# Kernel tuning notes

Measured on AMD Instinct MI355X. Metric: run time of the kernel, lower is better.

The kernel has to match this reference:

```python
import jax, jax.numpy as jnp
import numpy as np

# Genotype structure constants (see init_kwargs)
N_NODES = 100_000   # total nodes in topological order
N_IN = 1024         # first N_IN nodes are input-layer nodes (copy x)
N_OUT = 1024        # last N_OUT nodes are output-layer nodes
FAN_IN = 32         # predecessors per non-input node
BATCH = 128


def setup_inputs() -> dict:
    key = jax.random.key(0)
    k1, k2, k3 = jax.random.split(key, 3)
    x = jax.random.normal(k1, (BATCH, N_IN), dtype=jnp.float32)
    weights = jax.random.normal(k2, (N_NODES, FAN_IN), dtype=jnp.float32) * 0.5
    # predecessor ids: node i may only read nodes with index < i (topological DAG)
    raw = np.asarray(jax.random.randint(k3, (N_NODES, FAN_IN), 0, N_NODES))
    lim = np.maximum(np.arange(N_NODES), 1)[:, None]
    in_ids = jnp.asarray((raw % lim).astype(np.int32))
    return {"x": x, "weights": weights, "in_ids": in_ids}


def reference(x, weights, in_ids):
    B, n_in = x.shape
    n_nodes, _ = weights.shape
    # vals[i] holds the output of node i for every batch element: [N, B]
    vals = jnp.zeros((n_nodes, B), dtype=x.dtype).at[:n_in].set(x.T)
    node_idx = jnp.arange(n_in, n_nodes)

    def step(vals, inp):
        i, ids, w = inp
        gathered = vals[ids]                      # [K, B] predecessor outputs
        out = jax.nn.relu(jnp.einsum('k,kb->b', w, gathered))  # linear (no bias) + ReLU
        return vals.at[i].set(out), None

    vals, _ = jax.lax.scan(step, vals, (node_idx, in_ids[n_in:], weights[n_in:]))
    # stack output-layer node values -> [B, N_OUT]
    return vals[n_nodes - N_OUT:].T
```

## Files before the change

kernel.cpp:

```cpp
#include <hip/hip_runtime.h>
#include <hip/hip_fp16.h>


#define N_NODES 100000
#define N_IN    1024
#define N_OUT   1024
#define FAN_IN  32
#define NPAIR   64
#define N_TODO  (N_NODES - N_IN)
#define SENTW   0xFFFFFFFFu
#define NW      2048
#define NBLK    (NW / 4)
#define PGSZ    1024
#define PGSHIFT 10
#define NPAGES  ((N_TODO + PGSZ - 1) / PGSZ)

#define OFS_WM    4096
#define OFS_PC    8192
#define PC_STRIDE 64
#define OFS_VALS  65536

__global__ __launch_bounds__(256) void init_kernel(const float* __restrict__ x,
                                                   unsigned* __restrict__ vals,
                                                   int* __restrict__ wm_page,
                                                   int* __restrict__ page_cnt) {
    const int tid = blockIdx.x * blockDim.x + threadIdx.x;
    if (tid == 0) *wm_page = 0;
    if (tid < NPAGES) page_cnt[tid * PC_STRIDE] = 0;
    if (tid < N_IN * NPAIR) {
        const int i = tid >> 6;
        const int b = tid & 63;
        __half2 h2 = __floats2half2_rn(x[b * N_IN + i], x[(b + 64) * N_IN + i]);
        vals[i * NPAIR + b] = *reinterpret_cast<unsigned*>(&h2);
    }
    uint4* p = (uint4*)(vals + (size_t)N_IN * NPAIR);
    const int total = N_TODO * NPAIR / 4;
    const uint4 s4 = make_uint4(SENTW, SENTW, SENTW, SENTW);
    for (int t = tid; t < total; t += gridDim.x * blockDim.x)
        p[t] = s4;
}

__device__ __forceinline__ void wm_advance(int* wm_page, int* page_cnt) {
    for (;;) {
        int cur = __hip_atomic_load(wm_page, __ATOMIC_RELAXED,
                                    __HIP_MEMORY_SCOPE_AGENT);
        if (cur >= NPAGES) break;
        int fps = min(PGSZ, N_TODO - (cur << PGSHIFT));
        int cnt = __hip_atomic_load(page_cnt + (size_t)cur * PC_STRIDE,
                                    __ATOMIC_RELAXED, __HIP_MEMORY_SCOPE_AGENT);
        if (cnt < fps) break;
        int expected = cur;
        __hip_atomic_compare_exchange_strong(wm_page, &expected, cur + 1,
                                             __ATOMIC_RELAXED, __ATOMIC_RELAXED,
                                             __HIP_MEMORY_SCOPE_AGENT);
    }
}

__global__ __launch_bounds__(256, 2) void dag_kernel(const float* __restrict__ weights,
                                                     const int* __restrict__ in_ids,
                                                     unsigned* __restrict__ vals,
                                                     int* __restrict__ wm_page,
                                                     int* __restrict__ page_cnt,
                                                     float* __restrict__ out) {
    const int tid  = threadIdx.x;
    const int lane = tid & 63;
    const int w    = __builtin_amdgcn_readfirstlane(blockIdx.x * 4 + (tid >> 6));

    unsigned v[FAN_IN];
    unsigned vn[FAN_IN];
    unsigned wmv  = 0;
    unsigned cohm = 0, cmn = 0;
    int pend_pg = -1, pend_old = 0;

    int node = N_IN + w;

    {
        const long wb = (long)node * FAN_IN;
#pragma unroll
        for (int k = 0; k < FAN_IN; ++k) {
            const int id = in_ids[wb + k];
            const unsigned* p = vals + (long)id * NPAIR + lane;
            if (id < N_IN) {
                asm volatile("global_load_dword %0, %1, off"
                             : "=v"(vn[k]) : "v"(p));
            } else {
                asm volatile("global_load_dword %0, %1, off sc0 sc1"
                             : "=v"(vn[k]) : "v"(p));
                cmn |= 1u << k;
            }
        }
        asm volatile("global_load_dword %0, %1, off sc0 sc1"
                     : "=v"(wmv) : "v"(wm_page));
    }

    for (;;) {
        asm volatile("s_waitcnt vmcnt(0)" ::: "memory");
        __builtin_amdgcn_sched_barrier(0);

#pragma unroll
        for (int k = 0; k < FAN_IN; ++k) v[k] = vn[k];
        cohm = cmn;

        if (pend_pg >= 0) {
            if (lane == 0) {
                const int ps = min(PGSZ, N_TODO - (pend_pg << PGSHIFT));
                if (pend_old + 1 == ps) wm_advance(wm_page, page_cnt);
            }
            pend_pg = -1;
        }
        if (node - NW >= N_IN) {
            const int ppg = (node - NW - N_IN) >> PGSHIFT;
            if (lane == 0)
                pend_old = __hip_atomic_fetch_add(page_cnt + (size_t)ppg * PC_STRIDE, 1,
                                                  __ATOMIC_RELAXED,
                                                  __HIP_MEMORY_SCOPE_AGENT);
            pend_pg = ppg;
        }

        const int wmn = __builtin_amdgcn_readfirstlane((int)(N_IN + (wmv << PGSHIFT)));

        const int nxt = node + NW;
        cmn = 0;
        if (nxt < N_NODES) {
            const long wbn = (long)nxt * FAN_IN;
#pragma unroll
            for (int k = 0; k < FAN_IN; ++k) {
                const int id = in_ids[wbn + k];
                const unsigned* p = vals + (long)id * NPAIR + lane;
                if (id < wmn) {
                    asm volatile("global_load_dword %0, %1, off"
                                 : "=v"(vn[k]) : "v"(p));
                } else {
                    asm volatile("global_load_dword %0, %1, off sc0 sc1"
                                 : "=v"(vn[k]) : "v"(p));
                    cmn |= 1u << k;
                }
            }
            asm volatile("global_load_dword %0, %1, off sc0 sc1"
                         : "=v"(wmv) : "v"(wm_page));
        }

        const long wb = (long)node * FAN_IN;

        unsigned need = cohm;
        while (need) {
            unsigned got = 0;
#pragma unroll
            for (int k = 0; k < FAN_IN; ++k)
                if ((need >> k) & 1u)
                    if (__all(v[k] != SENTW)) got |= 1u << k;
            need &= ~got;
            if (!need) break;
            __builtin_amdgcn_s_sleep(1);
#pragma unroll
            for (int k = 0; k < FAN_IN; ++k)
                if ((need >> k) & 1u) {
                    const int id = in_ids[wb + k];
                    v[k] = __hip_atomic_load(vals + (long)id * NPAIR + lane,
                                             __ATOMIC_RELAXED,
                                             __HIP_MEMORY_SCOPE_AGENT);
                }
        }

        float acc0 = 0.f, acc1 = 0.f;
#pragma unroll
        for (int k = 0; k < FAN_IN; ++k) {
            const float  wk = weights[wb + k];
            const __half2 h2 = *reinterpret_cast<const __half2*>(&v[k]);
            const float2  f  = __half22float2(h2);
            acc0 = fmaf(wk, f.x, acc0);
            acc1 = fmaf(wk, f.y, acc1);
        }
        acc0 = fmaxf(acc0, 0.f);
        acc1 = fmaxf(acc1, 0.f);

        __half2 hr = __floats2half2_rn(acc0, acc1);
        const unsigned ow = *reinterpret_cast<const unsigned*>(&hr);
        unsigned* orow = vals + (long)node * NPAIR + lane;
        asm volatile("global_store_dword %0, %1, off sc0 sc1"
                     :: "v"(orow), "v"(ow));

        if (node >= N_NODES - N_OUT) {
            const int jo = node - (N_NODES - N_OUT);
            out[lane * N_OUT + jo]        = acc0;
            out[(lane + 64) * N_OUT + jo] = acc1;
        }

        if (nxt >= N_NODES) break;
        node = nxt;
    }

    asm volatile("s_waitcnt vmcnt(0)" ::: "memory");
    if (lane == 0) {
        if (pend_pg >= 0) {
            const int ps = min(PGSZ, N_TODO - (pend_pg << PGSHIFT));
            if (pend_old + 1 == ps) wm_advance(wm_page, page_cnt);
        }
        const int pg = (node - N_IN) >> PGSHIFT;
        const int ps = min(PGSZ, N_TODO - (pg << PGSHIFT));
        int old = __hip_atomic_fetch_add(page_cnt + (size_t)pg * PC_STRIDE, 1,
                                         __ATOMIC_RELAXED, __HIP_MEMORY_SCOPE_AGENT);
        if (old + 1 == ps) wm_advance(wm_page, page_cnt);
    }
}

extern "C" void kernel_launch(void* const* d_in, const int* in_sizes, int n_in,
                              void* d_out, int out_size, void* d_ws, size_t ws_size,
                              hipStream_t stream) {
    const float* x       = (const float*)d_in[0];
    const float* weights = (const float*)d_in[1];
    const int*   in_ids  = (const int*)d_in[2];
    float*       out     = (float*)d_out;

    int*      wm_page = (int*)((char*)d_ws + OFS_WM);
    int*      page_cnt= (int*)((char*)d_ws + OFS_PC);
    unsigned* vals    = (unsigned*)((char*)d_ws + OFS_VALS);

    init_kernel<<<2048, 256, 0, stream>>>(x, vals, wm_page, page_cnt);
    dag_kernel<<<NBLK, 256, 0, stream>>>(weights, in_ids, vals,
                                         wm_page, page_cnt, out);
}
```

Before: 564.5 us.

## Split page completion counters into sub-counters and replicate the watermark

Each page's single completion counter becomes 32 cache-line-padded sub-counters, one per wave group (w mod 32). A per-page subs_done counter records finished sub-counters, and the watermark advances only when all 32 are done. The watermark is also copied to 32 padded replicas that blocks poll by block index. This spreads atomic traffic and polling loads that all hit one address across many addresses. In exchange it adds a second atomic level, 31 extra stores on each watermark advance, and a larger workspace footprint.

New measurement: 524.7 us. -7.1%, faster.

```diff
diff --git a/kernel.cpp b/kernel.cpp
--- a/kernel.cpp
+++ b/kernel.cpp
@@ -14,19 +14,28 @@
 #define PGSZ    1024
 #define PGSHIFT 10
 #define NPAGES  ((N_TODO + PGSZ - 1) / PGSZ)
+#define NSUB    32
+#define WMREP   32
 
 #define OFS_WM    4096
-#define OFS_PC    8192
-#define PC_STRIDE 64
-#define OFS_VALS  65536
+#define OFS_SD    16384
+#define OFS_SUB   65536
+#define OFS_VALS  860160
+#define LSTRIDE   64
+
+__device__ __forceinline__ int subq(int pg) {
+    return min(PGSZ, N_TODO - (pg << PGSHIFT)) >> 5;
+}
 
 __global__ __launch_bounds__(256) void init_kernel(const float* __restrict__ x,
                                                    unsigned* __restrict__ vals,
-                                                   int* __restrict__ wm_page,
-                                                   int* __restrict__ page_cnt) {
+                                                   int* __restrict__ wm,
+                                                   int* __restrict__ subs_done,
+                                                   int* __restrict__ sub_cnt) {
     const int tid = blockIdx.x * blockDim.x + threadIdx.x;
-    if (tid == 0) *wm_page = 0;
-    if (tid < NPAGES) page_cnt[tid * PC_STRIDE] = 0;
+    if (tid < WMREP)        wm[tid * LSTRIDE] = 0;
+    if (tid < NPAGES)       subs_done[tid * LSTRIDE] = 0;
+    if (tid < NPAGES * NSUB) sub_cnt[tid * LSTRIDE] = 0;
     if (tid < N_IN * NPAIR) {
         const int i = tid >> 6;
         const int b = tid & 63;
@@ -40,31 +49,36 @@
         p[t] = s4;
 }
 
-__device__ __forceinline__ void wm_advance(int* wm_page, int* page_cnt) {
+__device__ __forceinline__ void wm_advance(int* wm, int* subs_done) {
     for (;;) {
-        int cur = __hip_atomic_load(wm_page, __ATOMIC_RELAXED,
-                                    __HIP_MEMORY_SCOPE_AGENT);
+        int cur = __hip_atomic_load(wm, __ATOMIC_RELAXED, __HIP_MEMORY_SCOPE_AGENT);
         if (cur >= NPAGES) break;
-        int fps = min(PGSZ, N_TODO - (cur << PGSHIFT));
-        int cnt = __hip_atomic_load(page_cnt + (size_t)cur * PC_STRIDE,
-                                    __ATOMIC_RELAXED, __HIP_MEMORY_SCOPE_AGENT);
-        if (cnt < fps) break;
+        int sd = __hip_atomic_load(subs_done + (size_t)cur * LSTRIDE,
+                                   __ATOMIC_RELAXED, __HIP_MEMORY_SCOPE_AGENT);
+        if (sd < NSUB) break;
         int expected = cur;
-        __hip_atomic_compare_exchange_strong(wm_page, &expected, cur + 1,
+        __hip_atomic_compare_exchange_strong(wm, &expected, cur + 1,
                                              __ATOMIC_RELAXED, __ATOMIC_RELAXED,
                                              __HIP_MEMORY_SCOPE_AGENT);
     }
+    int fin = __hip_atomic_load(wm, __ATOMIC_RELAXED, __HIP_MEMORY_SCOPE_AGENT);
+    for (int r = 1; r < WMREP; ++r)
+        __hip_atomic_store(wm + (size_t)r * LSTRIDE, fin,
+                           __ATOMIC_RELAXED, __HIP_MEMORY_SCOPE_AGENT);
 }
 
 __global__ __launch_bounds__(256, 2) void dag_kernel(const float* __restrict__ weights,
                                                      const int* __restrict__ in_ids,
                                                      unsigned* __restrict__ vals,
-                                                     int* __restrict__ wm_page,
-                                                     int* __restrict__ page_cnt,
+                                                     int* __restrict__ wm,
+                                                     int* __restrict__ subs_done,
+                                                     int* __restrict__ sub_cnt,
                                                      float* __restrict__ out) {
     const int tid  = threadIdx.x;
     const int lane = tid & 63;
     const int w    = __builtin_amdgcn_readfirstlane(blockIdx.x * 4 + (tid >> 6));
+    const int g    = w & (NSUB - 1);
+    int* wm_rep    = wm + (size_t)(blockIdx.x & (WMREP - 1)) * LSTRIDE;
 
     unsigned v[FAN_IN];
     unsigned vn[FAN_IN];
@@ -90,7 +104,7 @@
             }
         }
         asm volatile("global_load_dword %0, %1, off sc0 sc1"
-                     : "=v"(wmv) : "v"(wm_page));
+                     : "=v"(wmv) : "v"(wm_rep));
     }
 
     for (;;) {
@@ -102,18 +116,19 @@
         cohm = cmn;
 
         if (pend_pg >= 0) {
-            if (lane == 0) {
-                const int ps = min(PGSZ, N_TODO - (pend_pg << PGSHIFT));
-                if (pend_old + 1 == ps) wm_advance(wm_page, page_cnt);
+            if (lane == 0 && pend_old + 1 == subq(pend_pg)) {
+                int sd = __hip_atomic_fetch_add(subs_done + (size_t)pend_pg * LSTRIDE, 1,
+                                                __ATOMIC_RELAXED, __HIP_MEMORY_SCOPE_AGENT);
+                if (sd + 1 == NSUB) wm_advance(wm, subs_done);
             }
             pend_pg = -1;
         }
         if (node - NW >= N_IN) {
             const int ppg = (node - NW - N_IN) >> PGSHIFT;
             if (lane == 0)
-                pend_old = __hip_atomic_fetch_add(page_cnt + (size_t)ppg * PC_STRIDE, 1,
-                                                  __ATOMIC_RELAXED,
-                                                  __HIP_MEMORY_SCOPE_AGENT);
+                pend_old = __hip_atomic_fetch_add(
+                    sub_cnt + ((size_t)ppg * NSUB + g) * LSTRIDE, 1,
+                    __ATOMIC_RELAXED, __HIP_MEMORY_SCOPE_AGENT);
             pend_pg = ppg;
         }
 
@@ -137,7 +152,7 @@
                 }
             }
             asm volatile("global_load_dword %0, %1, off sc0 sc1"
-                         : "=v"(wmv) : "v"(wm_page));
+                         : "=v"(wmv) : "v"(wm_rep));
         }
 
         const long wb = (long)node * FAN_IN;
@@ -192,15 +207,19 @@
 
     asm volatile("s_waitcnt vmcnt(0)" ::: "memory");
     if (lane == 0) {
-        if (pend_pg >= 0) {
-            const int ps = min(PGSZ, N_TODO - (pend_pg << PGSHIFT));
-            if (pend_old + 1 == ps) wm_advance(wm_page, page_cnt);
+        if (pend_pg >= 0 && pend_old + 1 == subq(pend_pg)) {
+            int sd = __hip_atomic_fetch_add(subs_done + (size_t)pend_pg * LSTRIDE, 1,
+                                            __ATOMIC_RELAXED, __HIP_MEMORY_SCOPE_AGENT);
+            if (sd + 1 == NSUB) wm_advance(wm, subs_done);
         }
         const int pg = (node - N_IN) >> PGSHIFT;
-        const int ps = min(PGSZ, N_TODO - (pg << PGSHIFT));
-        int old = __hip_atomic_fetch_add(page_cnt + (size_t)pg * PC_STRIDE, 1,
+        int old = __hip_atomic_fetch_add(sub_cnt + ((size_t)pg * NSUB + g) * LSTRIDE, 1,
                                          __ATOMIC_RELAXED, __HIP_MEMORY_SCOPE_AGENT);
-        if (old + 1 == ps) wm_advance(wm_page, page_cnt);
+        if (old + 1 == subq(pg)) {
+            int sd = __hip_atomic_fetch_add(subs_done + (size_t)pg * LSTRIDE, 1,
+                                            __ATOMIC_RELAXED, __HIP_MEMORY_SCOPE_AGENT);
+            if (sd + 1 == NSUB) wm_advance(wm, subs_done);
+        }
     }
 }
 
@@ -212,11 +231,12 @@
     const int*   in_ids  = (const int*)d_in[2];
     float*       out     = (float*)d_out;
 
-    int*      wm_page = (int*)((char*)d_ws + OFS_WM);
-    int*      page_cnt= (int*)((char*)d_ws + OFS_PC);
-    unsigned* vals    = (unsigned*)((char*)d_ws + OFS_VALS);
-
-    init_kernel<<<2048, 256, 0, stream>>>(x, vals, wm_page, page_cnt);
+    int*      wm       = (int*)((char*)d_ws + OFS_WM);
+    int*      subs_done= (int*)((char*)d_ws + OFS_SD);
+    int*      sub_cnt  = (int*)((char*)d_ws + OFS_SUB);
+    unsigned* vals     = (unsigned*)((char*)d_ws + OFS_VALS);
+
+    init_kernel<<<2048, 256, 0, stream>>>(x, vals, wm, subs_done, sub_cnt);
     dag_kernel<<<NBLK, 256, 0, stream>>>(weights, in_ids, vals,
-                                         wm_page, page_cnt, out);
-}
+                                         wm, subs_done, sub_cnt, out);
+}
```
